# Kernel tuning notes

Hardware: AMD Instinct MI355X
Metric: run time of the kernel (lower is better)

The kernel has to match this reference:

```python
import jax, jax.numpy as jnp
import numpy as np

B, S, D, H = 2, 2048, 1024, 16
DK = D // H
EPS = 1e-5


def setup_inputs() -> dict:
    key = jax.random.key(0)
    ks = jax.random.split(key, 6)
    std = (2.0 / (D + D)) ** 0.5
    return {
        "x": jax.random.normal(ks[0], (B, S, D), dtype=jnp.float32),
        "W_Q": jax.random.normal(ks[1], (D, D), dtype=jnp.float32) * std,
        "W_K": jax.random.normal(ks[2], (D, D), dtype=jnp.float32) * std,
        "W_V": jax.random.normal(ks[3], (D, D), dtype=jnp.float32) * std,
        "W_O": jax.random.normal(ks[4], (D, D), dtype=jnp.float32) * std,
        "gain": jnp.ones((D,), dtype=jnp.float32),
        "positions": jnp.arange(S, dtype=jnp.int64 if jax.config.jax_enable_x64 else jnp.int32),
        "theta": 10000,
        "max_seq_len": 2048,
    }


def rmsnorm(x, gain):
    xf = x.astype(jnp.float32)
    rms = jnp.sqrt(jnp.mean(xf * xf, axis=-1, keepdims=True) + EPS)
    return ((xf / rms) * gain).astype(x.dtype)


def apply_rope(x, sin, cos):
    # x: [..., seq, dk]; sin/cos: [seq, dk//2] broadcast over leading dims
    x_even = x[..., 0::2]
    x_odd = x[..., 1::2]
    r_even = x_even * cos - x_odd * sin
    r_odd = x_odd * cos + x_even * sin
    return jnp.stack([r_even, r_odd], axis=-1).reshape(x.shape)


def reference(x, W_Q, W_K, W_V, W_O, gain, positions, theta, max_seq_len):
    seq_len = x.shape[-2]
    Q = jnp.einsum('od,bsd->bso', W_Q, x)
    K = jnp.einsum('od,bsd->bso', W_K, x)
    V = jnp.einsum('od,bsd->bso', W_V, x)
    # RMSNorm over full d_model BEFORE head split (as in original)
    Q = rmsnorm(Q, gain)
    K = rmsnorm(K, gain)
    # split heads: [b, h, s, dk]
    Q = Q.reshape(*Q.shape[:-1], H, DK).swapaxes(-3, -2)
    K = K.reshape(*K.shape[:-1], H, DK).swapaxes(-3, -2)
    V = V.reshape(*V.shape[:-1], H, DK).swapaxes(-3, -2)
    # RoPE tables
    exponents = 2.0 * jnp.arange(DK // 2, dtype=jnp.float32) / DK
    inv_freq = 1.0 / (jnp.float32(theta) ** exponents)
    angles = positions.astype(jnp.float32)[:, None] * inv_freq[None, :]  # [S, DK//2]
    sin, cos = jnp.sin(angles), jnp.cos(angles)
    Q = apply_rope(Q, sin, cos)
    K = apply_rope(K, sin, cos)
    # causal attention
    scores = jnp.einsum('bhqd,bhkd->bhqk', Q, K) / jnp.sqrt(jnp.float32(DK))
    causal = jnp.tril(jnp.ones((seq_len, seq_len), dtype=bool))
    scores = jnp.where(causal, scores, -jnp.inf)
    attn = jax.nn.softmax(scores, axis=-1)
    out = jnp.einsum('bhqk,bhkd->bhqd', attn, V)
    out = out.swapaxes(-3, -2).reshape(*x.shape[:-1], D)
    return jnp.einsum('of,bsf->bso', W_O, out)
```

## Files before the change

### kernel.cpp

```cpp
#include <hip/hip_runtime.h>
#include <hip/hip_bf16.h>

typedef __attribute__((ext_vector_type(8))) __bf16 bf16x8;
typedef __attribute__((ext_vector_type(4))) __bf16 bf16x4;
typedef __attribute__((ext_vector_type(4))) float  f32x4;
typedef __attribute__((ext_vector_type(4))) short  s16x4;

#define S_LEN 2048
#define D_DIM 1024
#define NH    16
#define GK    1024
#define GN    1024

__device__ __forceinline__ float fast_exp2(float x) {
#if __has_builtin(__builtin_amdgcn_exp2f)
  return __builtin_amdgcn_exp2f(x);
#else
  return exp2f(x);
#endif
}

__device__ __forceinline__ f32x4 mfma16(bf16x4 a, bf16x4 b, f32x4 c) {
#if __has_builtin(__builtin_amdgcn_mfma_f32_16x16x16_bf16)
  return __builtin_amdgcn_mfma_f32_16x16x16_bf16(a, b, c, 0, 0, 0);
#else
  return __builtin_amdgcn_mfma_f32_16x16x16bf16_1k(
      __builtin_bit_cast(s16x4, a), __builtin_bit_cast(s16x4, b), c, 0, 0, 0);
#endif
}

__device__ __forceinline__ void gld_lds16(const void* g, void* l) {
  __builtin_amdgcn_global_load_lds(
      (const __attribute__((address_space(1))) unsigned int*)g,
      (__attribute__((address_space(3))) unsigned int*)l, 16, 0, 0);
}

__global__ __launch_bounds__(256) void cast_all(
    const float* __restrict__ x,  const float* __restrict__ wq, const float* __restrict__ wk,
    const float* __restrict__ wv, const float* __restrict__ wo,
    __bf16* __restrict__ xb, __bf16* __restrict__ wqb, __bf16* __restrict__ wkb,
    __bf16* __restrict__ wvb, __bf16* __restrict__ wob)
{
  const int NTOT = 2 << 20;
  for (int i = blockIdx.x * 256 + threadIdx.x; i < NTOT; i += 1024 * 256) {
    const float* s; __bf16* d; int off;
    if (i < (1 << 20)) { s = x; d = xb; off = i; }
    else {
      const int j = i - (1 << 20);
      const int r = j >> 18; off = j & ((1 << 18) - 1);
      s = (r == 0) ? wq : (r == 1) ? wk : (r == 2) ? wv : wo;
      d = (r == 0) ? wqb : (r == 1) ? wkb : (r == 2) ? wvb : wob;
    }
    float4 v = ((const float4*)s)[off];
    bf16x4 o = { (__bf16)v.x, (__bf16)v.y, (__bf16)v.z, (__bf16)v.w };
    ((bf16x4*)d)[off] = o;
  }
}

__global__ __launch_bounds__(256, 3) void gemm_qkv(
    const __bf16* __restrict__ A,
    const __bf16* __restrict__ W0, const __bf16* __restrict__ W1, const __bf16* __restrict__ W2,
    __bf16* __restrict__ C0, __bf16* __restrict__ C1, __bf16* __restrict__ VtOut)
{
  const int bid = blockIdx.x;
  const int e = bid & 7, mg = e >> 1, ng = e & 1;
  const int q = bid >> 3;
  const int mt = mg * 8 + (q & 7);
  const int nt = ng * 12 + (q >> 3);
  const int mode = nt >> 3;
  const int m0 = mt * 128;
  const int n0 = (nt & 7) * 128;
  const __bf16* Wm = (mode == 0) ? W0 : (mode == 1) ? W1 : W2;

  __shared__ __align__(16) __bf16 As[128 * 64];
  __shared__ __align__(16) __bf16 Bs[128 * 64];

  const int tid  = threadIdx.x;
  const int lane = tid & 63;
  const int w    = tid >> 6;
  const int wr   = w >> 1, wc = w & 1;
  const int lm   = lane & 15, qd = lane >> 4;

  const __bf16* ap[4]; int loA[4];
  #pragma unroll
  for (int j = 0; j < 4; j++) {
    const int c = tid + 256 * j;
    const int r = c >> 3, cpos = c & 7;
    ap[j] = A + (size_t)(m0 + r) * GK + (cpos ^ (r & 7)) * 8;
    loA[j] = c * 8;
  }
  const __bf16* bp[4]; int loB[4];
  #pragma unroll
  for (int j = 0; j < 4; j++) {
    const int c = tid + 256 * j;
    const int r = c >> 3, cpos = c & 7;
    bp[j] = Wm + (size_t)(n0 + r) * GK + (cpos ^ (r & 7)) * 8;
    loB[j] = c * 8;
  }

  const int sw = lm & 7;

  f32x4 zero = {0.f, 0.f, 0.f, 0.f};
  f32x4 acc[4][4];
  #pragma unroll
  for (int i = 0; i < 4; i++)
    #pragma unroll
    for (int j = 0; j < 4; j++) acc[i][j] = zero;

  for (int k0 = 0; k0 < GK; k0 += 64) {
    #pragma unroll
    for (int j = 0; j < 4; j++) gld_lds16(ap[j] + k0, &As[loA[j]]);
    #pragma unroll
    for (int j = 0; j < 4; j++) gld_lds16(bp[j] + k0, &Bs[loB[j]]);
    __syncthreads();
    #pragma unroll
    for (int half = 0; half < 2; half++) {
      const int cph = ((qd + 4 * half) ^ sw) * 8;
      bf16x8 af[4], bfv[4];
      #pragma unroll
      for (int i = 0; i < 4; i++) af[i]  = *(const bf16x8*)&As[(wr * 64 + i * 16 + lm) * 64 + cph];
      #pragma unroll
      for (int j = 0; j < 4; j++) bfv[j] = *(const bf16x8*)&Bs[(wc * 64 + j * 16 + lm) * 64 + cph];
      #pragma unroll
      for (int i = 0; i < 4; i++)
        #pragma unroll
        for (int j = 0; j < 4; j++)
          acc[i][j] = __builtin_amdgcn_mfma_f32_16x16x32_bf16(af[i], bfv[j], acc[i][j], 0, 0, 0);
    }
    __syncthreads();
  }

  if (mode < 2) {
    __bf16* C = (mode == 0) ? C0 : C1;
    #pragma unroll
    for (int i = 0; i < 4; i++) {
      const int row = m0 + wr * 64 + i * 16 + qd * 4;
      #pragma unroll
      for (int j = 0; j < 4; j++) {
        const int col = n0 + wc * 64 + j * 16 + lm;
        #pragma unroll
        for (int r = 0; r < 4; r++)
          C[(size_t)(row + r) * GN + col] = (__bf16)acc[i][j][r];
      }
    }
  } else {
    #pragma unroll
    for (int i = 0; i < 4; i++) {
      const int row = m0 + wr * 64 + i * 16 + qd * 4;
      const int b = row >> 11, s = row & (S_LEN - 1);
      const int kt = s >> 6, kb = (s >> 4) & 3, qp = (s >> 2) & 3;
      #pragma unroll
      for (int j = 0; j < 4; j++) {
        const int col = n0 + wc * 64 + j * 16 + lm;
        const int h = col >> 6, d = col & 63;
        const int jb = d >> 4, lmv = d & 15;
        bf16x4 o = { (__bf16)acc[i][j][0], (__bf16)acc[i][j][1],
                     (__bf16)acc[i][j][2], (__bf16)acc[i][j][3] };
        const size_t idx =
            ((((size_t)((b * NH + h) * 32 + kt)) * 4 + kb) * 4 + jb) * 256 +
            (qp * 16 + lmv) * 4;
        *(bf16x4*)(VtOut + idx) = o;
      }
    }
  }
}

__global__ __launch_bounds__(256, 2) void gemm_out64(
    const __bf16* __restrict__ A, const __bf16* __restrict__ Wm, float* __restrict__ C)
{
  const int bid = blockIdx.x;
  const int e = bid & 7, mg = e >> 1, ng = e & 1;
  const int q = bid >> 3;
  const int m0 = (mg * 16 + (q & 15)) * 64;
  const int n0 = (ng * 4 + (q >> 4)) * 128;

  __shared__ __align__(16) __bf16 As[2][64 * 64];
  __shared__ __align__(16) __bf16 Bs[2][128 * 64];

  const int tid  = threadIdx.x;
  const int lane = tid & 63;
  const int w    = tid >> 6;
  const int wr   = w >> 1, wc = w & 1;
  const int lm   = lane & 15, qd = lane >> 4;

  const __bf16* ap[2]; int loA[2];
  #pragma unroll
  for (int j = 0; j < 2; j++) {
    const int c = tid + 256 * j;
    const int r = c >> 3, cpos = c & 7;
    ap[j] = A + (size_t)(m0 + r) * GK + (cpos ^ (r & 7)) * 8;
    loA[j] = c * 8;
  }
  const __bf16* bp[4]; int loB[4];
  #pragma unroll
  for (int j = 0; j < 4; j++) {
    const int c = tid + 256 * j;
    const int r = c >> 3, cpos = c & 7;
    bp[j] = Wm + (size_t)(n0 + r) * GK + (cpos ^ (r & 7)) * 8;
    loB[j] = c * 8;
  }

  const int sw = lm & 7;

  auto stage = [&](int buf, int k0) {
    #pragma unroll
    for (int j = 0; j < 2; j++) gld_lds16(ap[j] + k0, &As[buf][loA[j]]);
    #pragma unroll
    for (int j = 0; j < 4; j++) gld_lds16(bp[j] + k0, &Bs[buf][loB[j]]);
  };

  f32x4 zero = {0.f, 0.f, 0.f, 0.f};
  f32x4 acc[2][4];
  #pragma unroll
  for (int i = 0; i < 2; i++)
    #pragma unroll
    for (int j = 0; j < 4; j++) acc[i][j] = zero;

  stage(0, 0);

  for (int kt = 0; kt < 16; ++kt) {
    const int cur = kt & 1;
    __syncthreads();
    if (kt < 15) stage(cur ^ 1, (kt + 1) * 64);
    #pragma unroll
    for (int half = 0; half < 2; half++) {
      const int cph = ((qd + 4 * half) ^ sw) * 8;
      bf16x8 af[2], bfv[4];
      #pragma unroll
      for (int i = 0; i < 2; i++) af[i]  = *(const bf16x8*)&As[cur][(wr * 32 + i * 16 + lm) * 64 + cph];
      #pragma unroll
      for (int j = 0; j < 4; j++) bfv[j] = *(const bf16x8*)&Bs[cur][(wc * 64 + j * 16 + lm) * 64 + cph];
      #pragma unroll
      for (int i = 0; i < 2; i++)
        #pragma unroll
        for (int j = 0; j < 4; j++)
          acc[i][j] = __builtin_amdgcn_mfma_f32_16x16x32_bf16(af[i], bfv[j], acc[i][j], 0, 0, 0);
    }
  }

  #pragma unroll
  for (int i = 0; i < 2; i++) {
    const int row = m0 + wr * 32 + i * 16 + qd * 4;
    #pragma unroll
    for (int j = 0; j < 4; j++) {
      const int col = n0 + wc * 64 + j * 16 + lm;
      #pragma unroll
      for (int r = 0; r < 4; r++)
        C[(size_t)(row + r) * GN + col] = acc[i][j][r];
    }
  }
}

__global__ __launch_bounds__(256) void norm_rope(
    const __bf16* __restrict__ Qf, const __bf16* __restrict__ Kf,
    const float* __restrict__ gain, const int* __restrict__ positions,
    const int* __restrict__ theta_p,
    __bf16* __restrict__ Qh, __bf16* __restrict__ Kh)
{
  const int t = threadIdx.x;
  const int w = t >> 6, lane = t & 63;
  const int row = blockIdx.x * 4 + w;
  const int s = row & (S_LEN - 1), b = row >> 11;
  const int d0 = lane * 16;

  const bf16x8 qv0 = *(const bf16x8*)(Qf + (size_t)row * D_DIM + d0);
  const bf16x8 qv1 = *(const bf16x8*)(Qf + (size_t)row * D_DIM + d0 + 8);
  const bf16x8 kv0 = *(const bf16x8*)(Kf + (size_t)row * D_DIM + d0);
  const bf16x8 kv1 = *(const bf16x8*)(Kf + (size_t)row * D_DIM + d0 + 8);

  float q[16], k[16];
  #pragma unroll
  for (int j = 0; j < 8; j++) {
    q[j] = (float)qv0[j]; q[8 + j] = (float)qv1[j];
    k[j] = (float)kv0[j]; k[8 + j] = (float)kv1[j];
  }
  float sq = 0.f, sk = 0.f;
  #pragma unroll
  for (int j = 0; j < 16; j++) { sq += q[j] * q[j]; sk += k[j] * k[j]; }
  #pragma unroll
  for (int off = 32; off; off >>= 1) { sq += __shfl_xor(sq, off); sk += __shfl_xor(sk, off); }

  const float SC2 = 0.125f * 1.44269504089f;
  const float invq = rsqrtf(sq * (1.0f / 1024.0f) + 1e-5f) * SC2;
  const float invk = rsqrtf(sk * (1.0f / 1024.0f) + 1e-5f);

  float g[16];
  #pragma unroll
  for (int j = 0; j < 4; j++) {
    const float4 gv = *(const float4*)(gain + d0 + j * 4);
    g[4 * j] = gv.x; g[4 * j + 1] = gv.y; g[4 * j + 2] = gv.z; g[4 * j + 3] = gv.w;
  }

  const float pos  = (float)positions[s];
  const float lg32 = __log2f((float)theta_p[0]) * (1.0f / 32.0f);
  const int h = lane >> 2, idx0 = (lane & 3) * 16;

  bf16x8 qw0, qw1, kw0, kw1;
  #pragma unroll
  for (int pp = 0; pp < 8; pp++) {
    const int p = (lane & 3) * 8 + pp;
    const float f = fast_exp2(-(float)p * lg32);
    float sn, cs;
    __sincosf(pos * f, &sn, &cs);
    const float qe = q[2 * pp] * invq * g[2 * pp];
    const float qo = q[2 * pp + 1] * invq * g[2 * pp + 1];
    const float ke = k[2 * pp] * invk * g[2 * pp];
    const float ko = k[2 * pp + 1] * invk * g[2 * pp + 1];
    const __bf16 qre = (__bf16)(qe * cs - qo * sn);
    const __bf16 qro = (__bf16)(qo * cs + qe * sn);
    const __bf16 kre = (__bf16)(ke * cs - ko * sn);
    const __bf16 kro = (__bf16)(ko * cs + ke * sn);
    if (pp < 4) { qw0[2 * pp] = qre; qw0[2 * pp + 1] = qro;
                  kw0[2 * pp] = kre; kw0[2 * pp + 1] = kro; }
    else        { qw1[2 * (pp - 4)] = qre; qw1[2 * (pp - 4) + 1] = qro;
                  kw1[2 * (pp - 4)] = kre; kw1[2 * (pp - 4) + 1] = kro; }
  }

  const size_t obase = ((size_t)((b * NH + h) * S_LEN + s)) * 64 + idx0;
  *(bf16x8*)(Qh + obase)     = qw0;
  *(bf16x8*)(Qh + obase + 8) = qw1;
  *(bf16x8*)(Kh + obase)     = kw0;
  *(bf16x8*)(Kh + obase + 8) = kw1;
}

__global__ __launch_bounds__(256, 4) void attn_fwd(
    const __bf16* __restrict__ Qh, const __bf16* __restrict__ Kh,
    const __bf16* __restrict__ Vf, __bf16* __restrict__ Ob)
{
  const int bid = blockIdx.x;
  const int g   = bid >> 5, gj = g & 7, gs = g >> 3;
  const int qt  = (gs == 0) ? 31 - gj : (gs == 1) ? gj : (gs == 2) ? 23 - gj : 8 + gj;
  const int rr  = bid & 31;
  const int bh  = (rr & 7) * 4 + (rr >> 3);
  const int tid = threadIdx.x, lane = tid & 63, w = tid >> 6;
  const int lm = lane & 15, qd = lane >> 4;

  __shared__ __align__(16) __bf16 Ks[2][4096];

  const int row0 = qt * 64 + w * 16;
  const int qglob = row0 + lm;
  const size_t qbase = (size_t)bh * S_LEN * 64;
  const bf16x8 aq0 = *(const bf16x8*)(Qh + qbase + (size_t)qglob * 64 + qd * 8);
  const bf16x8 aq1 = *(const bf16x8*)(Qh + qbase + (size_t)qglob * 64 + 32 + qd * 8);

  const __bf16* Kb = Kh + (size_t)bh * S_LEN * 64;
  const __bf16* Vbh = Vf + (size_t)bh * 32 * 4096;
  const int c0 = tid, c1 = 256 + tid;
  const int kr0 = c0 >> 3, kr1 = c1 >> 3;
  const int kg0 = ((c0 & 7) ^ (kr0 & 7)) * 8;
  const int kg1 = ((c1 & 7) ^ (kr1 & 7)) * 8;
  const int cpA = (qd ^ (lm & 7)) * 8;
  const int cpB = cpA ^ 32;

  auto stage = [&](int buf, int k0) {
    gld_lds16(Kb + (size_t)(k0 + kr0) * 64 + kg0, &Ks[buf][c0 * 8]);
    gld_lds16(Kb + (size_t)(k0 + kr1) * 64 + kg1, &Ks[buf][c1 * 8]);
  };

  f32x4 zero = {0.f, 0.f, 0.f, 0.f};
  f32x4 lacc = zero;
  f32x4 o[4];
  #pragma unroll
  for (int jb = 0; jb < 4; jb++) o[jb] = zero;

  bf16x4 ones4;
  #pragma unroll
  for (int i = 0; i < 4; i++) ones4[i] = (__bf16)1.0f;

  stage(0, 0);

  for (int kt = 0; kt <= qt; ++kt) {
    const int cur = kt & 1;
    __syncthreads();
    if (kt < qt) stage(cur ^ 1, (kt + 1) * 64);

    const __bf16* Vtile = Vbh + (size_t)kt * 4096;
    bf16x4 av[4][4];
    #pragma unroll
    for (int kb = 0; kb < 4; kb++)
      #pragma unroll
      for (int jb = 0; jb < 4; jb++)
        av[kb][jb] = *(const bf16x4*)(Vtile + ((kb * 4 + jb) * 64 + lane) * 4);

    const __bf16* Kc = &Ks[cur][0];
    const int k0 = kt * 64;
    const bool diag = (kt == qt);

    bf16x4 pfrag[4];
    #pragma unroll
    for (int kb = 0; kb < 4; kb++) {
      const int krow = (kb * 16 + lm) * 64;
      const bf16x8 ak0 = *(const bf16x8*)&Kc[krow + cpA];
      const bf16x8 ak1 = *(const bf16x8*)&Kc[krow + cpB];
      f32x4 sc = zero;
      sc = __builtin_amdgcn_mfma_f32_16x16x32_bf16(ak0, aq0, sc, 0, 0, 0);
      sc = __builtin_amdgcn_mfma_f32_16x16x32_bf16(ak1, aq1, sc, 0, 0, 0);
      float p[4];
      if (diag) {
        const int keyb = k0 + kb * 16 + qd * 4;
        #pragma unroll
        for (int r = 0; r < 4; r++)
          p[r] = (keyb + r <= qglob) ? fast_exp2(sc[r]) : 0.f;
      } else {
        #pragma unroll
        for (int r = 0; r < 4; r++) p[r] = fast_exp2(sc[r]);
      }
      bf16x4 pf = { (__bf16)p[0], (__bf16)p[1], (__bf16)p[2], (__bf16)p[3] };
      pfrag[kb] = pf;
      lacc = mfma16(ones4, pf, lacc);
    }

    #pragma unroll
    for (int jb = 0; jb < 4; jb++)
      #pragma unroll
      for (int kb = 0; kb < 4; kb++)
        o[jb] = mfma16(av[kb][jb], pfrag[kb], o[jb]);
  }

  const int b = bh >> 4, h = bh & 15;
  const float inv = 1.0f / lacc[0];
  const size_t base = ((size_t)(b * S_LEN + qglob)) * D_DIM + h * 64 + qd * 4;
  #pragma unroll
  for (int jb = 0; jb < 4; jb++) {
    bf16x4 ov = { (__bf16)(o[jb][0] * inv), (__bf16)(o[jb][1] * inv),
                  (__bf16)(o[jb][2] * inv), (__bf16)(o[jb][3] * inv) };
    *(bf16x4*)(Ob + base + jb * 16) = ov;
  }
}

extern "C" void kernel_launch(void* const* d_in, const int* in_sizes, int n_in,
                              void* d_out, int out_size, void* d_ws, size_t ws_size,
                              hipStream_t stream)
{
  (void)in_sizes; (void)n_in; (void)out_size; (void)ws_size;
  const float* x    = (const float*)d_in[0];
  const float* WQ   = (const float*)d_in[1];
  const float* WK   = (const float*)d_in[2];
  const float* WV   = (const float*)d_in[3];
  const float* WO   = (const float*)d_in[4];
  const float* gain = (const float*)d_in[5];
  const int* positions = (const int*)d_in[6];
  const int* theta     = (const int*)d_in[7];
  float* out = (float*)d_out;

  char* ws = (char*)d_ws;
  const size_t MB = 1024 * 1024;
  __bf16* xb  = (__bf16*)(ws + 0);
  __bf16* WQb = (__bf16*)(ws + 8  * MB);
  __bf16* WKb = (__bf16*)(ws + 10 * MB);
  __bf16* WVb = (__bf16*)(ws + 12 * MB);
  __bf16* WOb = (__bf16*)(ws + 14 * MB);
  __bf16* Qfb = (__bf16*)(ws + 16 * MB);
  __bf16* Kfb = (__bf16*)(ws + 24 * MB);
  __bf16* Vf  = (__bf16*)(ws + 32 * MB);
  __bf16* Qh  = (__bf16*)(ws + 40 * MB);
  __bf16* Kh  = (__bf16*)(ws + 48 * MB);
  __bf16* Ob  = (__bf16*)(ws + 56 * MB);

  cast_all<<<1024, 256, 0, stream>>>(x, WQ, WK, WV, WO, xb, WQb, WKb, WVb, WOb);
  gemm_qkv<<<768, 256, 0, stream>>>(xb, WQb, WKb, WVb, Qfb, Kfb, Vf);
  norm_rope<<<1024, 256, 0, stream>>>(Qfb, Kfb, gain, positions, theta, Qh, Kh);
  attn_fwd<<<1024, 256, 0, stream>>>(Qh, Kh, Vf, Ob);
  gemm_out64<<<512, 256, 0, stream>>>(Ob, WOb, out);
}
```

Baseline: 192.2 us.

## Prefetch next V tile into registers with ping-pong buffers and wider loads

The V-fragment layout written by the projection GEMM is changed so that each lane's two adjacent jb blocks sit contiguously, which lets the attention kernel issue 8-element loads instead of 4-element ones. The attention loop is unrolled by two with ping-pong register sets, so V for tile kt+1 is loaded from global memory while tile kt is computed. This is meant to hide global-load latency for V behind the MFMA work and to halve the number of V load instructions. In exchange it uses more VGPRs, which could hurt occupancy under launch_bounds(256,2).

```diff
diff --git a/kernel.cpp b/kernel.cpp
--- a/kernel.cpp
+++ b/kernel.cpp
@@ -157,8 +157,8 @@
         bf16x4 o = { (__bf16)acc[i][j][0], (__bf16)acc[i][j][1],
                      (__bf16)acc[i][j][2], (__bf16)acc[i][j][3] };
         const size_t idx =
-            ((((size_t)((b * NH + h) * 32 + kt)) * 4 + kb) * 4 + jb) * 256 +
-            (qp * 16 + lmv) * 4;
+            (((size_t)((b * NH + h) * 32 + kt)) * 8 + (kb * 2 + (jb >> 1))) * 512 +
+            (qp * 16 + lmv) * 8 + (jb & 1) * 4;
         *(bf16x4*)(VtOut + idx) = o;
       }
     }
@@ -343,7 +343,7 @@
   const bf16x8 aq0 = *(const bf16x8*)(Qh + qbase + (size_t)qglob * 64 + qd * 8);
   const bf16x8 aq1 = *(const bf16x8*)(Qh + qbase + (size_t)qglob * 64 + 32 + qd * 8);
 
-  const __bf16* Kb = Kh + (size_t)bh * S_LEN * 64;
+  const __bf16* Kb  = Kh + (size_t)bh * S_LEN * 64;
   const __bf16* Vbh = Vf + (size_t)bh * 32 * 4096;
   const int c0 = tid, c1 = 256 + tid;
   const int kr0 = c0 >> 3, kr1 = c1 >> 3;
@@ -367,55 +367,74 @@
   #pragma unroll
   for (int i = 0; i < 4; i++) ones4[i] = (__bf16)1.0f;
 
+  bf16x8 avpX[4][2], avpY[4][2];
+
+#define LOADV(AVP, KT)                                                       \
+  {                                                                          \
+    const __bf16* vt_ = Vbh + (size_t)(KT) * 4096;                           \
+    _Pragma("unroll")                                                        \
+    for (int kb_ = 0; kb_ < 4; kb_++)                                        \
+      _Pragma("unroll")                                                      \
+      for (int jp_ = 0; jp_ < 2; jp_++)                                      \
+        AVP[kb_][jp_] = *(const bf16x8*)(vt_ + (kb_ * 2 + jp_) * 512 + lane * 8); \
+  }
+
+#define BODY(AVP, KT)                                                        \
+  {                                                                          \
+    const __bf16* Kc = &Ks[(KT) & 1][0];                                     \
+    const int k0_ = (KT) * 64;                                               \
+    const bool diag = ((KT) == qt);                                          \
+    bf16x4 pfrag[4];                                                         \
+    _Pragma("unroll")                                                        \
+    for (int kb_ = 0; kb_ < 4; kb_++) {                                      \
+      const int krow = (kb_ * 16 + lm) * 64;                                 \
+      const bf16x8 ak0 = *(const bf16x8*)&Kc[krow + cpA];                    \
+      const bf16x8 ak1 = *(const bf16x8*)&Kc[krow + cpB];                    \
+      f32x4 sc = zero;                                                       \
+      sc = __builtin_amdgcn_mfma_f32_16x16x32_bf16(ak0, aq0, sc, 0, 0, 0);   \
+      sc = __builtin_amdgcn_mfma_f32_16x16x32_bf16(ak1, aq1, sc, 0, 0, 0);   \
+      float p[4];                                                            \
+      if (diag) {                                                            \
+        const int keyb = k0_ + kb_ * 16 + qd * 4;                            \
+        _Pragma("unroll")                                                    \
+        for (int r = 0; r < 4; r++)                                          \
+          p[r] = (keyb + r <= qglob) ? fast_exp2(sc[r]) : 0.f;               \
+      } else {                                                               \
+        _Pragma("unroll")                                                    \
+        for (int r = 0; r < 4; r++) p[r] = fast_exp2(sc[r]);                 \
+      }                                                                      \
+      bf16x4 pf = { (__bf16)p[0], (__bf16)p[1], (__bf16)p[2], (__bf16)p[3] };\
+      pfrag[kb_] = pf;                                                       \
+      lacc = mfma16(ones4, pf, lacc);                                        \
+    }                                                                        \
+    _Pragma("unroll")                                                        \
+    for (int jb_ = 0; jb_ < 4; jb_++)                                        \
+      _Pragma("unroll")                                                      \
+      for (int kb_ = 0; kb_ < 4; kb_++) {                                    \
+        const bf16x8 vv = AVP[kb_][jb_ >> 1];                                \
+        bf16x4 av;                                                           \
+        if (jb_ & 1) { av[0] = vv[4]; av[1] = vv[5]; av[2] = vv[6]; av[3] = vv[7]; } \
+        else         { av[0] = vv[0]; av[1] = vv[1]; av[2] = vv[2]; av[3] = vv[3]; } \
+        o[jb_] = mfma16(av, pfrag[kb_], o[jb_]);                             \
+      }                                                                      \
+  }
+
   stage(0, 0);
-
-  for (int kt = 0; kt <= qt; ++kt) {
-    const int cur = kt & 1;
+  LOADV(avpX, 0);
+
+  for (int kt = 0; kt <= qt; ) {
     __syncthreads();
-    if (kt < qt) stage(cur ^ 1, (kt + 1) * 64);
-
-    const __bf16* Vtile = Vbh + (size_t)kt * 4096;
-    bf16x4 av[4][4];
-    #pragma unroll
-    for (int kb = 0; kb < 4; kb++)
-      #pragma unroll
-      for (int jb = 0; jb < 4; jb++)
-        av[kb][jb] = *(const bf16x4*)(Vtile + ((kb * 4 + jb) * 64 + lane) * 4);
-
-    const __bf16* Kc = &Ks[cur][0];
-    const int k0 = kt * 64;
-    const bool diag = (kt == qt);
-
-    bf16x4 pfrag[4];
-    #pragma unroll
-    for (int kb = 0; kb < 4; kb++) {
-      const int krow = (kb * 16 + lm) * 64;
-      const bf16x8 ak0 = *(const bf16x8*)&Kc[krow + cpA];
-      const bf16x8 ak1 = *(const bf16x8*)&Kc[krow + cpB];
-      f32x4 sc = zero;
-      sc = __builtin_amdgcn_mfma_f32_16x16x32_bf16(ak0, aq0, sc, 0, 0, 0);
-      sc = __builtin_amdgcn_mfma_f32_16x16x32_bf16(ak1, aq1, sc, 0, 0, 0);
-      float p[4];
-      if (diag) {
-        const int keyb = k0 + kb * 16 + qd * 4;
-        #pragma unroll
-        for (int r = 0; r < 4; r++)
-          p[r] = (keyb + r <= qglob) ? fast_exp2(sc[r]) : 0.f;
-      } else {
-        #pragma unroll
-        for (int r = 0; r < 4; r++) p[r] = fast_exp2(sc[r]);
-      }
-      bf16x4 pf = { (__bf16)p[0], (__bf16)p[1], (__bf16)p[2], (__bf16)p[3] };
-      pfrag[kb] = pf;
-      lacc = mfma16(ones4, pf, lacc);
-    }
-
-    #pragma unroll
-    for (int jb = 0; jb < 4; jb++)
-      #pragma unroll
-      for (int kb = 0; kb < 4; kb++)
-        o[jb] = mfma16(av[kb][jb], pfrag[kb], o[jb]);
-  }
+    if (kt < qt) { stage((kt + 1) & 1, (kt + 1) * 64); LOADV(avpY, kt + 1); }
+    BODY(avpX, kt);
+    ++kt;
+    if (kt > qt) break;
+    __syncthreads();
+    if (kt < qt) { stage((kt + 1) & 1, (kt + 1) * 64); LOADV(avpX, kt + 1); }
+    BODY(avpY, kt);
+    ++kt;
+  }
+#undef LOADV
+#undef BODY
 
   const int b = bh >> 4, h = bh & 15;
   const float inv = 1.0f / lacc[0];
```

Result: slower. 207.1 us (+7.8%).
